# Kernel tuning notes

Measured on AMD Instinct MI355X. Metric: run time of the kernel, lower is better.

The kernel has to match this reference:

```python
import jax, jax.numpy as jnp
import numpy as np

NUM_HEADS = 16
NEG_INF = -1e30


def setup_inputs() -> dict:
    key = jax.random.key(0)
    k1, k2, k3 = jax.random.split(key, 3)
    B, S, D = 2, 2048, 1024
    x = jax.random.normal(k1, (B, S, D), dtype=jnp.float32)
    # torch Linear(D, 3D, bias=False) stored here already transposed: y = x @ w_qkv
    w_qkv = jax.random.normal(k2, (D, 3 * D), dtype=jnp.float32) * 0.02
    w_out = jax.random.normal(k3, (D, D), dtype=jnp.float32) * 0.02
    return {"x": x, "w_qkv": w_qkv, "w_out": w_out}


def reference(x, w_qkv, w_out):
    B, S, D = x.shape
    H = NUM_HEADS
    dh = D // H
    qkv = x @ w_qkv                      # [B, S, 3D]
    q, k, v = jnp.split(qkv, 3, axis=-1)

    def to_heads(t):
        return t.reshape(B, S, H, dh).transpose(0, 2, 1, 3)  # [B, H, S, dh]

    q, k, v = to_heads(q), to_heads(k), to_heads(v)
    scale = jnp.asarray(dh, x.dtype) ** -0.5
    scores = jnp.einsum('bhqd,bhkd->bhqk', q, k) * scale     # [B, H, S, S]
    causal = jnp.tril(jnp.ones((S, S), dtype=bool))
    scores = jnp.where(causal, scores, NEG_INF)
    attn = jax.nn.softmax(scores, axis=-1)
    out = jnp.einsum('bhqk,bhkd->bhqd', attn, v)             # [B, H, S, dh]
    out = out.transpose(0, 2, 1, 3).reshape(B, S, D)
    return out @ w_out
```

## Files before the change

### kernel.cpp

```cpp
#include <hip/hip_runtime.h>

typedef unsigned short u16;
typedef unsigned int u32;

typedef __bf16 bf16x8 __attribute__((ext_vector_type(8)));
typedef _Float16 f16x8 __attribute__((ext_vector_type(8)));
typedef float f32x4 __attribute__((ext_vector_type(4)));

typedef __attribute__((address_space(1))) u32 as1_u32;
typedef __attribute__((address_space(3))) u32 as3_u32;

#define EKF 0.18033688011112042f

__device__ __forceinline__ u16 f2bf(float x) {
  u32 u = __float_as_uint(x);
  u = u + 0x7fffu + ((u >> 16) & 1u);
  return (u16)(u >> 16);
}
__device__ __forceinline__ u32 pack2(float a, float b) {
  return (u32)f2bf(a) | ((u32)f2bf(b) << 16);
}
__device__ __forceinline__ u32 pkf16(float a, float b) {
  return __builtin_bit_cast(u32, __builtin_amdgcn_cvt_pkrtz(a, b));
}
__device__ __forceinline__ u16 f2h(float a) {
  return (u16)(pkf16(a, a) & 0xffffu);
}
__device__ __forceinline__ void gld_lds16(const u16* g, const u16* l) {
  __builtin_amdgcn_global_load_lds((const as1_u32*)g, (as3_u32*)l, 16, 0, 0);
}

__global__ __launch_bounds__(256) void prepass_kernel(const float* __restrict__ x,
                                                      const float* __restrict__ w_qkv,
                                                      const float* __restrict__ w_out,
                                                      u16* __restrict__ xb,
                                                      u16* __restrict__ wqkvT,
                                                      u16* __restrict__ woutT) {
  __shared__ float tile[64][65];
  int bid = blockIdx.x;
  int t = threadIdx.x;
  if (bid < 4096) {
    int i = bid * 256 + t;
    float4 v = ((const float4*)x)[i];
    uint2 r;
    r.x = pack2(v.x, v.y);
    r.y = pack2(v.z, v.w);
    ((uint2*)xb)[i] = r;
    return;
  }
  const float* W;
  u16* WT;
  int K, N, bx, by;
  if (bid < 4096 + 768) {
    int b2 = bid - 4096;
    W = w_qkv; WT = wqkvT; K = 1024; N = 3072; bx = b2 & 15; by = b2 >> 4;
  } else {
    int b2 = bid - 4864;
    W = w_out; WT = woutT; K = 1024; N = 1024; bx = b2 & 15; by = b2 >> 4;
  }
  int k0 = bx * 64, n0 = by * 64;
  int r = t >> 4, c4 = (t & 15) * 4;
#pragma unroll
  for (int i = 0; i < 4; ++i) {
    int row = r + i * 16;
    float4 v = *(const float4*)&W[(size_t)(k0 + row) * N + n0 + c4];
    tile[row][c4 + 0] = v.x; tile[row][c4 + 1] = v.y;
    tile[row][c4 + 2] = v.z; tile[row][c4 + 3] = v.w;
  }
  __syncthreads();
#pragma unroll
  for (int i = 0; i < 4; ++i) {
    int n = r + i * 16;
    uint2 o;
    o.x = pack2(tile[c4 + 0][n], tile[c4 + 1][n]);
    o.y = pack2(tile[c4 + 2][n], tile[c4 + 3][n]);
    *(uint2*)&WT[(size_t)(n0 + n) * K + k0 + c4] = o;
  }
}

template <int OUT_MODE, int BN>
__global__ __launch_bounds__(256) void gemm_bt_kernel(const u16* __restrict__ A,
                                                      const u16* __restrict__ BT,
                                                      void* __restrict__ Cv,
                                                      u16* __restrict__ VT,
                                                      int M, int N, int K) {
  const int NF = (BN == 128) ? 4 : 2;
  __shared__ __attribute__((aligned(16))) u16 sA[128 * 64];
  __shared__ __attribute__((aligned(16))) u16 sB[BN * 64];
  const int tid = threadIdx.x;
  const int wave = tid >> 6;
  const int lane = tid & 63;
  const int bm = blockIdx.y * 128;
  const int bn = blockIdx.x * BN;
  const int wm = (wave >> 1) * 64;
  const int wn = (wave & 1) * (BN / 2);
  const int lr = lane & 15;
  const int kg = lane >> 4;
  const int lr7 = lr & 7;

  const int sr = tid >> 3;
  const int sc = tid & 7;
  const int scg = (sc ^ (sr & 7)) * 8;
  const u16* pa = A + (size_t)(bm + sr) * K + scg;
  const u16* pb = BT + (size_t)(bn + sr) * K + scg;
  const u16* la = sA + wave * 512;
  const u16* lb = sB + wave * 512;

  f32x4 acc[4][NF];
#pragma unroll
  for (int i = 0; i < 4; i++)
#pragma unroll
    for (int j = 0; j < NF; j++) {
      f32x4 z = {0.f, 0.f, 0.f, 0.f};
      acc[i][j] = z;
    }

  for (int k0 = 0; k0 < K; k0 += 64) {
    __syncthreads();
#pragma unroll
    for (int i = 0; i < 4; ++i)
      gld_lds16(pa + (size_t)(i * 32) * K + k0, la + i * 2048);
#pragma unroll
    for (int i = 0; i < NF; ++i)
      gld_lds16(pb + (size_t)(i * 32) * K + k0, lb + i * 2048);
    __syncthreads();
#pragma unroll
    for (int kk = 0; kk < 2; ++kk) {
      bf16x8 af[4], bfr[NF];
      const int ch = ((kk * 4 + kg) ^ lr7) * 8;
#pragma unroll
      for (int mi = 0; mi < 4; mi++)
        af[mi] = *(const bf16x8*)(sA + (wm + mi * 16 + lr) * 64 + ch);
#pragma unroll
      for (int ni = 0; ni < NF; ni++)
        bfr[ni] = *(const bf16x8*)(sB + (wn + ni * 16 + lr) * 64 + ch);
#pragma unroll
      for (int mi = 0; mi < 4; mi++)
#pragma unroll
        for (int ni = 0; ni < NF; ni++)
          acc[mi][ni] = __builtin_amdgcn_mfma_f32_16x16x32_bf16(bfr[ni], af[mi], acc[mi][ni], 0, 0, 0);
    }
  }

  if (OUT_MODE == 0) {
    float* buf = (float*)sA;
    float* outp = (float*)Cv;
#pragma unroll
    for (int hc = 0; hc < 2; ++hc) {
      __syncthreads();
      if ((wave & 1) == hc) {
#pragma unroll
        for (int mi = 0; mi < 4; mi++)
#pragma unroll
          for (int ni = 0; ni < NF; ni++) {
            int row = wm + mi * 16 + lr;
            int cp = ((ni * 4 + kg) ^ lr7) * 4;
            *(f32x4*)(buf + row * 32 + cp) = acc[mi][ni];
          }
      }
      __syncthreads();
#pragma unroll
      for (int i = 0; i < 4; ++i) {
        int row = i * 32 + (tid >> 3);
        int lc = tid & 7;
        float4 v = *(const float4*)(buf + row * 32 + ((lc ^ (row & 7)) * 4));
        *(float4*)(outp + (size_t)(bm + row) * N + bn + hc * 32 + lc * 4) = v;
      }
    }
  } else if (bn >= 2048) {
#pragma unroll
    for (int mi = 0; mi < 4; mi++)
#pragma unroll
      for (int ni = 0; ni < NF; ni++) {
        int r = bm + wm + mi * 16 + lr;
        int cc = bn + wn + ni * 16 + kg * 4 - 2048;
        int bh2 = (r >> 11) * 16 + (cc >> 6);
        int j = r & 2047;
        u16* vrow = VT + ((size_t)bh2 * 64 + (cc & 63)) * 2048 + j;
        f32x4 a = acc[mi][ni];
#pragma unroll
        for (int rr = 0; rr < 4; rr++)
          vrow[(size_t)rr * 2048] = f2h(a[rr]);
      }
  } else {
    float scale = (bn < 1024) ? EKF : 1.0f;
    u16* buf = sA;
    u16* qkp = (u16*)Cv;
#pragma unroll
    for (int hc = 0; hc < 2; ++hc) {
      __syncthreads();
      if ((wave & 1) == hc) {
#pragma unroll
        for (int mi = 0; mi < 4; mi++)
#pragma unroll
          for (int ni = 0; ni < NF; ni++) {
            int row = wm + mi * 16 + lr;
            int sp = ((ni * 4 + kg) ^ (lr & 6)) * 4;
            f32x4 a = acc[mi][ni];
            *(uint2*)(buf + row * 64 + sp) =
                make_uint2(pack2(a[0] * scale, a[1] * scale),
                           pack2(a[2] * scale, a[3] * scale));
          }
      }
      __syncthreads();
#pragma unroll
      for (int i = 0; i < 4; ++i) {
        int row = i * 32 + (tid >> 3);
        int lc = tid & 7;
        uint4 v = *(const uint4*)(buf + row * 64 + (((2 * lc) ^ (row & 6)) * 4));
        *(uint4*)(qkp + (size_t)(bm + row) * 2048 + bn + hc * 64 + lc * 8) = v;
      }
    }
  }
}

__global__ __launch_bounds__(256, 4) void attn_mfma_kernel(const u16* __restrict__ qk,
                                                           const u16* __restrict__ vt,
                                                           u16* __restrict__ out) {
  __shared__ __attribute__((aligned(16))) u16 sK[2][64 * 64];
  __shared__ __attribute__((aligned(16))) u16 sV[2][64 * 64];
  __shared__ __attribute__((aligned(16))) u16 sP[4][16 * 64];

  const int tid = threadIdx.x;
  const int wave = tid >> 6;
  const int lane = tid & 63;
  const int lr = lane & 15;
  const int kg = lane >> 4;
  const int l7 = lr & 7;

  int idx = blockIdx.x;
  int qi = 31 - (idx >> 5);
  int bh = idx & 31;
  int b = bh >> 4, h = bh & 15;
  int q0 = qi * 64;

  const u16* qbase = qk + (size_t)b * 2048 * 2048 + h * 64;
  const u16* kbase = qbase + 1024;
  const u16* vbase = vt + (size_t)bh * 64 * 2048;
  u16* obase = out + (size_t)b * 2048 * 1024 + h * 64;

  const int sra = wave * 16 + (lane >> 3);
  const int srb = sra + 8;
  const int sc = lane & 7;
  const u32 koffA = (u32)sra * 2048 + (u32)((sc ^ (sra & 7)) * 8);
  const u32 koffB = (u32)srb * 2048 + (u32)((sc ^ (srb & 7)) * 8);
  const u32 ldsA = (wave * 2 + 0) * 512;
  const u32 ldsB = (wave * 2 + 1) * 512;

  const int qcol = q0 + wave * 16 + lr;
  bf16x8 qf0, qf1;
  {
    const u16* qrow = qbase + (size_t)qcol * 2048;
    qf0 = *(const bf16x8*)(qrow + kg * 8);
    qf1 = *(const bf16x8*)(qrow + 32 + kg * 8);
  }

  const u32 ka0 = (u32)(lr * 64 + ((kg ^ l7) * 8));
  const u32 ka1 = (u32)(lr * 64 + (((4 + kg) ^ l7) * 8));
  u16* const sPw = sP[wave];
  const u32 pr0 = (u32)(lr * 64 + (((kg * 2) ^ (l7 << 1)) * 4));
  const u32 pr1 = (u32)(lr * 64 + (((8 + kg * 2) ^ (l7 << 1)) * 4));

  f32x4 oacc[4];
#pragma unroll
  for (int i = 0; i < 4; ++i) {
    f32x4 z = {0.f, 0.f, 0.f, 0.f};
    oacc[i] = z;
  }
  float lsum = 0.f;

  const int nrounds = qi + 1;
  gld_lds16(kbase + koffA, sK[0] + ldsA);
  gld_lds16(kbase + koffB, sK[0] + ldsB);
  gld_lds16(vbase + koffA, sV[0] + ldsA);
  gld_lds16(vbase + koffB, sV[0] + ldsB);
  __syncthreads();

  for (int t = 0; t < nrounds; ++t) {
    if (t + 1 < nrounds) {
      int j1 = (t + 1) * 64;
      u16* dK = sK[(t + 1) & 1];
      u16* dV = sV[(t + 1) & 1];
      gld_lds16(kbase + (size_t)j1 * 2048 + koffA, dK + ldsA);
      gld_lds16(kbase + (size_t)j1 * 2048 + koffB, dK + ldsB);
      gld_lds16(vbase + j1 + koffA, dV + ldsA);
      gld_lds16(vbase + j1 + koffB, dV + ldsB);
    }
    const u16* sKb = sK[t & 1];
    const u16* sVb = sV[t & 1];
    const bool diag = (t == qi);

#pragma unroll
    for (int jt = 0; jt < 4; ++jt) {
      u16* pw = sPw + lr * 64 + (((jt * 4 + kg) ^ (l7 << 1)) * 4);
      if (!diag || jt <= wave) {
        bf16x8 kf0 = *(const bf16x8*)(sKb + jt * 1024 + ka0);
        bf16x8 kf1 = *(const bf16x8*)(sKb + jt * 1024 + ka1);
        f32x4 c = {0.f, 0.f, 0.f, 0.f};
        c = __builtin_amdgcn_mfma_f32_16x16x32_bf16(kf0, qf0, c, 0, 0, 0);
        c = __builtin_amdgcn_mfma_f32_16x16x32_bf16(kf1, qf1, c, 0, 0, 0);
        float p0 = exp2f(c[0]);
        float p1 = exp2f(c[1]);
        float p2 = exp2f(c[2]);
        float p3 = exp2f(c[3]);
        if (diag && jt == wave) {
          int jr = kg * 4;
          p0 = (jr + 0 <= lr) ? p0 : 0.f;
          p1 = (jr + 1 <= lr) ? p1 : 0.f;
          p2 = (jr + 2 <= lr) ? p2 : 0.f;
          p3 = (jr + 3 <= lr) ? p3 : 0.f;
        }
        lsum += (p0 + p1) + (p2 + p3);
        *(uint2*)pw = make_uint2(pkf16(p0, p1), pkf16(p2, p3));
      } else {
        *(uint2*)pw = make_uint2(0u, 0u);
      }
    }

    asm volatile("" ::: "memory");

    f16x8 pf0 = *(const f16x8*)(sPw + pr0);
    f16x8 pf1 = *(const f16x8*)(sPw + pr1);
#pragma unroll
    for (int dt = 0; dt < 4; ++dt) {
      f16x8 vf0 = *(const f16x8*)(sVb + dt * 1024 + ka0);
      f16x8 vf1 = *(const f16x8*)(sVb + dt * 1024 + ka1);
      oacc[dt] = __builtin_amdgcn_mfma_f32_16x16x32_f16(vf0, pf0, oacc[dt], 0, 0, 0);
      oacc[dt] = __builtin_amdgcn_mfma_f32_16x16x32_f16(vf1, pf1, oacc[dt], 0, 0, 0);
    }
    __syncthreads();
  }

  lsum += __shfl_xor(lsum, 16);
  lsum += __shfl_xor(lsum, 32);
  float inv = 1.0f / lsum;

  u16* orow = obase + (size_t)qcol * 1024;
#pragma unroll
  for (int dt = 0; dt < 4; ++dt) {
    uint2 o2 = make_uint2(pack2(oacc[dt][0] * inv, oacc[dt][1] * inv),
                          pack2(oacc[dt][2] * inv, oacc[dt][3] * inv));
    *(uint2*)(orow + dt * 16 + kg * 4) = o2;
  }
}

extern "C" void kernel_launch(void* const* d_in, const int* in_sizes, int n_in,
                              void* d_out, int out_size, void* d_ws, size_t ws_size,
                              hipStream_t stream) {
  const float* x = (const float*)d_in[0];
  const float* w_qkv = (const float*)d_in[1];
  const float* w_out = (const float*)d_in[2];
  float* out = (float*)d_out;

  char* ws = (char*)d_ws;
  u16* xb    = (u16*)(ws);
  u16* wqkvT = (u16*)(ws + (8u << 20));
  u16* woutT = (u16*)(ws + (14u << 20));
  u16* qkb   = (u16*)(ws + (16u << 20));
  u16* vtb   = (u16*)(ws + (32u << 20));
  u16* attn  = (u16*)(ws + (40u << 20));

  prepass_kernel<<<5120, 256, 0, stream>>>(x, w_qkv, w_out, xb, wqkvT, woutT);

  gemm_bt_kernel<2, 128><<<dim3(3072 / 128, 4096 / 128), 256, 0, stream>>>(
      xb, wqkvT, (void*)qkb, vtb, 4096, 3072, 1024);

  attn_mfma_kernel<<<1024, 256, 0, stream>>>(qkb, vtb, attn);

  gemm_bt_kernel<0, 64><<<dim3(1024 / 64, 4096 / 128), 256, 0, stream>>>(
      attn, woutT, (void*)out, nullptr, 4096, 1024, 1024);
}
```

Measured before the change: 174.3 us.

## Add dedicated 256x256-tile QKV GEMM kernel with LDS double buffering

Replaces the generic 128x128 QKV projection GEMM with a specialized 512-thread kernel that computes 256x256 output tiles. It uses double-buffered direct global-to-LDS loads with an XOR swizzle, a block-index swizzle for L2 locality, and staged LDS stores for coalesced Q/K output. The aim is more data reuse per loaded tile and overlap of loads with MFMA work. The trade-off is only 192 blocks on a large-CU GPU, so occupancy is lower and wave quantization may be uneven.

```diff
diff --git a/kernel.cpp b/kernel.cpp
--- a/kernel.cpp
+++ b/kernel.cpp
@@ -75,6 +75,130 @@
     o.x = pack2(tile[c4 + 0][n], tile[c4 + 1][n]);
     o.y = pack2(tile[c4 + 2][n], tile[c4 + 3][n]);
     *(uint2*)&WT[(size_t)(n0 + n) * K + k0 + c4] = o;
+  }
+}
+
+__global__ __launch_bounds__(512, 2) void gemm_qkv256_kernel(const u16* __restrict__ A,
+                                                             const u16* __restrict__ BT,
+                                                             u16* __restrict__ QK,
+                                                             u16* __restrict__ VT) {
+  __shared__ __attribute__((aligned(16))) u16 smem[65536];
+  const int tid = threadIdx.x;
+  const int wave = tid >> 6;
+  const int lane = tid & 63;
+  const int lr = lane & 15;
+  const int kg = lane >> 4;
+  const int l7 = lr & 7;
+  const int wr = wave >> 2;
+  const int wc = wave & 3;
+
+  int b = blockIdx.x;
+  int sw = (b & 7) * 24 + (b >> 3);
+  const int bn = (sw % 12) * 256;
+  const int bm = (sw / 12) * 256;
+
+  const int srow = tid >> 3;
+  const int scg = ((tid & 7) ^ (srow & 7)) * 8;
+  const u16* pa = A + (size_t)(bm + srow) * 1024 + scg;
+  const u16* pb = BT + (size_t)(bn + srow) * 1024 + scg;
+  const u32 lw = (u32)wave * 512;
+
+  f32x4 acc[8][4];
+#pragma unroll
+  for (int i = 0; i < 8; ++i)
+#pragma unroll
+    for (int j = 0; j < 4; ++j) {
+      f32x4 z = {0.f, 0.f, 0.f, 0.f};
+      acc[i][j] = z;
+    }
+
+  {
+    u16* dA = (u16*)smem;
+    u16* dB = (u16*)smem + 16384;
+#pragma unroll
+    for (int i = 0; i < 4; ++i) gld_lds16(pa + (size_t)(i * 64) * 1024, dA + lw + i * 4096);
+#pragma unroll
+    for (int i = 0; i < 4; ++i) gld_lds16(pb + (size_t)(i * 64) * 1024, dB + lw + i * 4096);
+  }
+
+  for (int t = 0; t < 16; ++t) {
+    __syncthreads();
+    const u16* bA = smem + (t & 1) * 32768;
+    const u16* bB = bA + 16384;
+    if (t + 1 < 16) {
+      u16* dA = (u16*)smem + ((t + 1) & 1) * 32768;
+      u16* dB = dA + 16384;
+      const int k1 = (t + 1) * 64;
+#pragma unroll
+      for (int i = 0; i < 4; ++i) gld_lds16(pa + (size_t)(i * 64) * 1024 + k1, dA + lw + i * 4096);
+#pragma unroll
+      for (int i = 0; i < 4; ++i) gld_lds16(pb + (size_t)(i * 64) * 1024 + k1, dB + lw + i * 4096);
+    }
+    bf16x8 bfr[2][4];
+#pragma unroll
+    for (int kh = 0; kh < 2; ++kh)
+#pragma unroll
+      for (int ni = 0; ni < 4; ++ni)
+        bfr[kh][ni] = *(const bf16x8*)(bB + (wc * 64 + ni * 16 + lr) * 64 +
+                                       (((kh * 4 + kg) ^ l7) * 8));
+#pragma unroll
+    for (int ph = 0; ph < 4; ++ph) {
+      const int mh = ph >> 1, kh = ph & 1;
+      bf16x8 af[4];
+#pragma unroll
+      for (int mi = 0; mi < 4; ++mi)
+        af[mi] = *(const bf16x8*)(bA + (wr * 128 + mh * 64 + mi * 16 + lr) * 64 +
+                                  (((kh * 4 + kg) ^ l7) * 8));
+      __builtin_amdgcn_s_barrier();
+      __builtin_amdgcn_s_setprio(1);
+#pragma unroll
+      for (int mi = 0; mi < 4; ++mi)
+#pragma unroll
+        for (int ni = 0; ni < 4; ++ni)
+          acc[mh * 4 + mi][ni] = __builtin_amdgcn_mfma_f32_16x16x32_bf16(
+              bfr[kh][ni], af[mi], acc[mh * 4 + mi][ni], 0, 0, 0);
+      __builtin_amdgcn_s_setprio(0);
+      __builtin_amdgcn_s_barrier();
+    }
+  }
+
+  __syncthreads();
+  if (bn >= 2048) {
+#pragma unroll
+    for (int mi = 0; mi < 8; ++mi)
+#pragma unroll
+      for (int ni = 0; ni < 4; ++ni) {
+        int r = bm + wr * 128 + mi * 16 + lr;
+        int c = bn + wc * 64 + ni * 16 + kg * 4 - 2048;
+        int bh2 = (r >> 11) * 16 + (c >> 6);
+        int j = r & 2047;
+        u16* vrow = VT + ((size_t)bh2 * 64 + (c & 63)) * 2048 + j;
+        f32x4 a = acc[mi][ni];
+#pragma unroll
+        for (int rr = 0; rr < 4; ++rr) vrow[(size_t)rr * 2048] = f2h(a[rr]);
+      }
+  } else {
+    float scale = (bn < 1024) ? EKF : 1.0f;
+#pragma unroll
+    for (int mi = 0; mi < 8; ++mi)
+#pragma unroll
+      for (int ni = 0; ni < 4; ++ni) {
+        int row = wr * 128 + mi * 16 + lr;
+        u32 off = (u32)row * 256 + wc * 64 + (((ni * 4 + kg) ^ (lr & 6)) * 4);
+        f32x4 a = acc[mi][ni];
+        *(uint2*)((u16*)smem + off) =
+            make_uint2(pack2(a[0] * scale, a[1] * scale), pack2(a[2] * scale, a[3] * scale));
+      }
+    __syncthreads();
+#pragma unroll
+    for (int i = 0; i < 16; ++i) {
+      int row = i * 16 + (tid >> 5);
+      int lc = tid & 31;
+      int blk = lc >> 3, cc = lc & 7;
+      uint4 v = *(const uint4*)((const u16*)smem + (u32)row * 256 + blk * 64 +
+                                (((2 * cc) ^ (row & 6)) * 4));
+      *(uint4*)(QK + (size_t)(bm + row) * 2048 + bn + blk * 64 + cc * 8) = v;
+    }
   }
 }
 
@@ -362,8 +486,7 @@
 
   prepass_kernel<<<5120, 256, 0, stream>>>(x, w_qkv, w_out, xb, wqkvT, woutT);
 
-  gemm_bt_kernel<2, 128><<<dim3(3072 / 128, 4096 / 128), 256, 0, stream>>>(
-      xb, wqkvT, (void*)qkb, vtb, 4096, 3072, 1024);
+  gemm_qkv256_kernel<<<192, 512, 0, stream>>>(xb, wqkvT, qkb, vtb);
 
   attn_mfma_kernel<<<1024, 256, 0, stream>>>(qkb, vtb, attn);
 
```

Result: faster. 169.0 us (-3.0%).
